# Optimization experiments

Measured on AMD Instinct MI355X. Metric: run time of the kernel, lower is better.

The kernel has to match this reference:

```python
import jax, jax.numpy as jnp
import numpy as np

N = 100000
HEADS = 4
NHID = 32


def _gat_conv(x, src, dst, W, a_src, a_dst, b):
    # x: [N, Fin]; src/dst: [E'] (self-loops already appended)
    h = (x @ W).reshape(N, HEADS, NHID)                      # [N, H, D]
    al_src = jnp.einsum('nhd,hd->nh', h, a_src)              # [N, H]
    al_dst = jnp.einsum('nhd,hd->nh', h, a_dst)
    e = jax.nn.leaky_relu(al_src[src] + al_dst[dst], 0.2)    # [E', H]
    # segment softmax over incoming edges of each destination node
    m = jax.ops.segment_max(e, dst, num_segments=N)          # [N, H]
    ex = jnp.exp(e - m[dst])
    s = jax.ops.segment_sum(ex, dst, num_segments=N)         # [N, H]
    alpha = ex / (s[dst] + 1e-16)                            # [E', H]
    msg = h[src] * alpha[:, :, None]                         # [E', H, D]
    out = jax.ops.segment_sum(msg, dst, num_segments=N)      # [N, H, D]
    return out.reshape(N, HEADS * NHID) + b


def setup_inputs() -> dict:
    key = jax.random.key(0)
    ks = jax.random.split(key, 16)
    E = 1600000
    NFEAT, NCLASS = 128, 10
    width = HEADS * NHID  # 128
    sc = 0.1
    inp = {
        'x': jax.random.normal(ks[0], (N, NFEAT), jnp.float32),
        'edge_index': jax.random.randint(ks[1], (2, E), 0, N, jnp.int64)
            if jax.config.jax_enable_x64 else jax.random.randint(ks[1], (2, E), 0, N, jnp.int32),
        'W0': jax.random.normal(ks[2], (NFEAT, width), jnp.float32) * sc,
        'a_src0': jax.random.normal(ks[3], (HEADS, NHID), jnp.float32) * sc,
        'a_dst0': jax.random.normal(ks[4], (HEADS, NHID), jnp.float32) * sc,
        'b0': jnp.zeros((width,), jnp.float32),
        'W1': jax.random.normal(ks[5], (width, width), jnp.float32) * sc,
        'a_src1': jax.random.normal(ks[6], (HEADS, NHID), jnp.float32) * sc,
        'a_dst1': jax.random.normal(ks[7], (HEADS, NHID), jnp.float32) * sc,
        'b1': jnp.zeros((width,), jnp.float32),
        'W2': jax.random.normal(ks[8], (width, width), jnp.float32) * sc,
        'a_src2': jax.random.normal(ks[9], (HEADS, NHID), jnp.float32) * sc,
        'a_dst2': jax.random.normal(ks[10], (HEADS, NHID), jnp.float32) * sc,
        'b2': jnp.zeros((width,), jnp.float32),
        'fc_W': jax.random.normal(ks[11], (width, NCLASS), jnp.float32) * sc,
        'fc_b': jnp.zeros((NCLASS,), jnp.float32),
    }
    return inp


def reference(x, edge_index, W0, a_src0, a_dst0, b0, W1, a_src1, a_dst1, b1,
              W2, a_src2, a_dst2, b2, fc_W, fc_b):
    # PyG GATConv default add_self_loops=True
    loops = jnp.arange(N, dtype=edge_index.dtype)
    src = jnp.concatenate([edge_index[0], loops])
    dst = jnp.concatenate([edge_index[1], loops])
    h = x
    for (W, a_s, a_d, b) in ((W0, a_src0, a_dst0, b0),
                             (W1, a_src1, a_dst1, b1),
                             (W2, a_src2, a_dst2, b2)):
        h = jax.nn.elu(_gat_conv(h, src, dst, W, a_s, a_d, b))
        # F.dropout(training=False) -> identity
    logits = h @ fc_W + fc_b
    return jax.nn.log_softmax(logits, axis=1)
```

## Files before the change

kernel.cpp:

```cpp
#include <hip/hip_runtime.h>
#include <math.h>

#define NN 100000
#define FEAT 128
#define NHEAD 4
#define BSH 9
#define BNODES 512
#define NBUCK 196
#define BCAP 16384
#define PA_EPT 16
#define GTILES 6250
#define HSTRIDE 136

typedef unsigned int uint;
typedef unsigned short ushort;
typedef __attribute__((ext_vector_type(8))) short short8;
typedef __attribute__((ext_vector_type(4))) float fx4;

__device__ __forceinline__ float lrelu(float v) { return v > 0.f ? v : 0.2f * v; }

__device__ __forceinline__ ushort f2bf(float f) {
    uint u = __float_as_uint(f);
    return (ushort)((u + 0x7fffu + ((u >> 16) & 1u)) >> 16);
}
__device__ __forceinline__ float bf_lo(uint u) { return __uint_as_float(u << 16); }
__device__ __forceinline__ float bf_hi(uint u) { return __uint_as_float(u & 0xffff0000u); }

__global__ __launch_bounds__(256) void convert_bf_kernel(
    const float* __restrict__ x, ushort* __restrict__ xbf)
{
    int i = blockIdx.x * 256 + threadIdx.x;
    if (i >= NN * FEAT / 4) return;
    float4 v = ((const float4*)x)[i];
    ushort4 u;
    u.x = f2bf(v.x); u.y = f2bf(v.y); u.z = f2bf(v.z); u.w = f2bf(v.w);
    ((ushort4*)xbf)[i] = u;
}

__global__ __launch_bounds__(256, 2) void gemm_mfma_kernel(
    const ushort* __restrict__ inbf, const float* __restrict__ W,
    const float* __restrict__ a_src, const float* __restrict__ a_dst,
    ushort* __restrict__ hbf, float* __restrict__ al_s, float* __restrict__ al_d)
{
    __shared__ __align__(16) ushort WA[FEAT * FEAT];
    __shared__ __align__(16) ushort HS[4][16 * HSTRIDE];
    const int t = threadIdx.x;
    for (int idx = t; idx < FEAT * FEAT; idx += 256) {
        int k = idx >> 7, m = idx & 127;
        int mt = m >> 4, kt = k >> 5, qq = (k >> 3) & 3, j = k & 7;
        int ln = qq * 16 + (m & 15);
        WA[((mt * 4 + kt) * 64 + ln) * 8 + j] = f2bf(W[idx]);
    }
    __syncthreads();

    const int wv = t >> 6, lane = t & 63;
    const int node_l = lane & 15, q = lane >> 4;

    short8 afr[8][4];
    #pragma unroll
    for (int mt = 0; mt < 8; ++mt)
        #pragma unroll
        for (int kt = 0; kt < 4; ++kt)
            afr[mt][kt] = *(const short8*)&WA[((mt * 4 + kt) * 64 + lane) * 8];

    const int stride = gridDim.x * 4;
    int tile = blockIdx.x * 4 + wv;
    if (tile >= GTILES) return;

    const ushort* rowp = inbf + (size_t)(tile * 16 + node_l) * FEAT + q * 8;
    short8 b0 = *(const short8*)(rowp);
    short8 b1 = *(const short8*)(rowp + 32);
    short8 b2 = *(const short8*)(rowp + 64);
    short8 b3 = *(const short8*)(rowp + 96);

    for (; tile < GTILES; tile += stride) {
        const int n0 = tile * 16;
        int ntile = tile + stride;
        short8 nb0, nb1, nb2, nb3;
        if (ntile < GTILES) {
            const ushort* nrp = inbf + (size_t)(ntile * 16 + node_l) * FEAT + q * 8;
            nb0 = *(const short8*)(nrp);
            nb1 = *(const short8*)(nrp + 32);
            nb2 = *(const short8*)(nrp + 64);
            nb3 = *(const short8*)(nrp + 96);
        }
        fx4 zero = {0.f, 0.f, 0.f, 0.f};
        fx4 acc[8];
        #pragma unroll
        for (int mt = 0; mt < 8; ++mt) acc[mt] = zero;
        #pragma unroll
        for (int kt = 0; kt < 4; ++kt) {
            short8 b = (kt == 0) ? b0 : (kt == 1) ? b1 : (kt == 2) ? b2 : b3;
            #pragma unroll
            for (int mt = 0; mt < 8; ++mt)
                acc[mt] = __builtin_amdgcn_mfma_f32_16x16x32_bf16(afr[mt][kt], b, acc[mt], 0, 0, 0);
        }
        float ps[4] = {0.f, 0.f, 0.f, 0.f};
        float pd[4] = {0.f, 0.f, 0.f, 0.f};
        #pragma unroll
        for (int mt = 0; mt < 8; ++mt) {
            float4 as4 = *(const float4*)(a_src + mt * 16 + q * 4);
            float4 ad4 = *(const float4*)(a_dst + mt * 16 + q * 4);
            ps[mt >> 1] += acc[mt][0] * as4.x + acc[mt][1] * as4.y + acc[mt][2] * as4.z + acc[mt][3] * as4.w;
            pd[mt >> 1] += acc[mt][0] * ad4.x + acc[mt][1] * ad4.y + acc[mt][2] * ad4.z + acc[mt][3] * ad4.w;
            ushort4 hv;
            hv.x = f2bf(acc[mt][0]); hv.y = f2bf(acc[mt][1]);
            hv.z = f2bf(acc[mt][2]); hv.w = f2bf(acc[mt][3]);
            *(ushort4*)&HS[wv][node_l * HSTRIDE + mt * 16 + q * 4] = hv;
        }
        #pragma unroll
        for (int h = 0; h < 4; ++h) {
            ps[h] += __shfl_xor(ps[h], 16); ps[h] += __shfl_xor(ps[h], 32);
            pd[h] += __shfl_xor(pd[h], 16); pd[h] += __shfl_xor(pd[h], 32);
        }
        float vs = (q == 0) ? ps[0] : (q == 1) ? ps[1] : (q == 2) ? ps[2] : ps[3];
        float vd = (q == 0) ? pd[0] : (q == 1) ? pd[1] : (q == 2) ? pd[2] : pd[3];
        al_s[(n0 + node_l) * 4 + q] = vs;
        al_d[(n0 + node_l) * 4 + q] = vd;
        #pragma unroll
        for (int it = 0; it < 4; ++it) {
            int fi = it * 64 + lane;
            int row = fi >> 4, colc = fi & 15;
            short8 v = *(const short8*)&HS[wv][row * HSTRIDE + colc * 8];
            *(short8*)(hbf + (size_t)n0 * FEAT + (size_t)fi * 8) = v;
        }
        b0 = nb0; b1 = nb1; b2 = nb2; b3 = nb3;
    }
}


__global__ void zero_small_kernel(int* bsize)
{
    int t = threadIdx.x;
    if (t < NBUCK) bsize[t] = 0;
}

__global__ __launch_bounds__(256) void bucket_hist_kernel(
    const int* __restrict__ ei, int E, int* bsize)
{
    __shared__ int lh[NBUCK];
    int t = threadIdx.x;
    if (t < NBUCK) lh[t] = 0;
    __syncthreads();
    int stride = gridDim.x * 256;
    for (int i = blockIdx.x * 256 + t; i < E + NN; i += stride) {
        int d = (i < E) ? ei[E + i] : (i - E);
        atomicAdd(&lh[d >> BSH], 1);
    }
    __syncthreads();
    if (t < NBUCK && lh[t]) atomicAdd(&bsize[t], lh[t]);
}

__global__ __launch_bounds__(256) void bucket_scan_kernel(
    const int* __restrict__ bsize, int* bbase, int* bcursor)
{
    __shared__ int sm[256];
    int t = threadIdx.x;
    int v = (t < NBUCK) ? bsize[t] : 0;
    sm[t] = v;
    __syncthreads();
    #pragma unroll
    for (int off = 1; off < 256; off <<= 1) {
        int x = (t >= off) ? sm[t - off] : 0;
        __syncthreads();
        sm[t] += x;
        __syncthreads();
    }
    if (t < NBUCK) {
        int excl = sm[t] - v;
        bbase[t] = excl;
        bcursor[t] = excl;
    }
    if (t == 255) bbase[NBUCK] = sm[255];
}

__global__ __launch_bounds__(256) void phaseA_bin_kernel(
    const int* __restrict__ ei, int E, int* bcursor, int2* __restrict__ pairs)
{
    __shared__ int lh[NBUCK], lb[NBUCK];
    int t = threadIdx.x;
    if (t < NBUCK) lh[t] = 0;
    __syncthreads();
    int base = blockIdx.x * (256 * PA_EPT) + t;
    int s[PA_EPT], d[PA_EPT];
    #pragma unroll
    for (int k = 0; k < PA_EPT; ++k) {
        int i = base + k * 256;
        if (i < E)            { s[k] = ei[i]; d[k] = ei[E + i]; }
        else if (i < E + NN)  { s[k] = i - E; d[k] = s[k]; }
        else                  { s[k] = 0; d[k] = -1; }
        if (d[k] >= 0) atomicAdd(&lh[d[k] >> BSH], 1);
    }
    __syncthreads();
    if (t < NBUCK) {
        int c = lh[t];
        lb[t] = c ? atomicAdd(&bcursor[t], c) : 0;
        lh[t] = 0;
    }
    __syncthreads();
    #pragma unroll
    for (int k = 0; k < PA_EPT; ++k) {
        if (d[k] >= 0) {
            int b = d[k] >> BSH;
            int off = atomicAdd(&lh[b], 1);
            pairs[lb[b] + off] = make_int2(d[k], s[k]);
        }
    }
}

__global__ __launch_bounds__(256) void phaseB_kernel(
    const int2* __restrict__ pairs, const int* __restrict__ bbase,
    int* __restrict__ row_ptr, int* __restrict__ colidx, int EP)
{
    __shared__ int nh[BNODES];
    __shared__ int ex[BNODES];
    __shared__ int ss[256];
    __shared__ int img[BCAP];
    int b = blockIdx.x, t = threadIdx.x;
    int node0 = b << BSH;
    int nend = min(NN - node0, BNODES);
    int pb = bbase[b], pe = bbase[b + 1];
    int span = pe - pb;
    for (int j = t; j < BNODES; j += 256) nh[j] = 0;
    __syncthreads();
    for (int i = t; i < span; i += 256)
        atomicAdd(&nh[pairs[pb + i].x - node0], 1);
    __syncthreads();
    int v0 = nh[2 * t], v1 = nh[2 * t + 1];
    int psc = v0 + v1;
    ss[t] = psc;
    __syncthreads();
    #pragma unroll
    for (int off = 1; off < 256; off <<= 1) {
        int x = (t >= off) ? ss[t - off] : 0;
        __syncthreads();
        ss[t] += x;
        __syncthreads();
    }
    int ep = ss[t] - psc;
    ex[2 * t] = ep;
    ex[2 * t + 1] = ep + v0;
    __syncthreads();
    for (int j = t; j < nend; j += 256) row_ptr[node0 + j] = pb + ex[j];
    if (b == NBUCK - 1 && t == 0) row_ptr[NN] = EP;
    for (int j = t; j < BNODES; j += 256) nh[j] = ex[j];
    __syncthreads();
    if (span <= BCAP) {
        for (int i = t; i < span; i += 256) {
            int2 p = pairs[pb + i];
            int pos = atomicAdd(&nh[p.x - node0], 1);
            img[pos] = p.y;
        }
        __syncthreads();
        for (int i = t; i < span; i += 256) colidx[pb + i] = img[i];
    } else {
        for (int i = t; i < span; i += 256) {
            int2 p = pairs[pb + i];
            int pos = atomicAdd(&nh[p.x - node0], 1);
            colidx[pb + pos] = p.y;
        }
    }
}

#define AGGR_STEP(hv, wgt)                                                    \
    a0 = fmaf(wgt, bf_lo(hv.x), a0); a1 = fmaf(wgt, bf_hi(hv.x), a1);        \
    a2 = fmaf(wgt, bf_lo(hv.y), a2); a3 = fmaf(wgt, bf_hi(hv.y), a3);        \
    a4 = fmaf(wgt, bf_lo(hv.z), a4); a5 = fmaf(wgt, bf_hi(hv.z), a5);        \
    a6 = fmaf(wgt, bf_lo(hv.w), a6); a7 = fmaf(wgt, bf_hi(hv.w), a7);

#define PROC4(cv)                                                             \
    {                                                                         \
        int s0 = cv.x, s1 = cv.y, s2 = cv.z, s3 = cv.w;                       \
        float w0 = __expf(lrelu(al_s[s0*4 + head] + ald_h));                  \
        float w1 = __expf(lrelu(al_s[s1*4 + head] + ald_h));                  \
        float w2 = __expf(lrelu(al_s[s2*4 + head] + ald_h));                  \
        float w3 = __expf(lrelu(al_s[s3*4 + head] + ald_h));                  \
        uint4 h0 = ((const uint4*)(hbf + (size_t)s0 * FEAT))[lane];           \
        uint4 h1 = ((const uint4*)(hbf + (size_t)s1 * FEAT))[lane];           \
        uint4 h2 = ((const uint4*)(hbf + (size_t)s2 * FEAT))[lane];           \
        uint4 h3 = ((const uint4*)(hbf + (size_t)s3 * FEAT))[lane];           \
        ssum += (w0 + w1) + (w2 + w3);                                        \
        AGGR_STEP(h0, w0) AGGR_STEP(h1, w1) AGGR_STEP(h2, w2) AGGR_STEP(h3, w3) \
    }

__global__ __launch_bounds__(256) void aggr_csr_kernel(
    const int* __restrict__ row_ptr, const int* __restrict__ colidx,
    const ushort* __restrict__ hbf, const float* __restrict__ al_s,
    const float* __restrict__ al_d, const float* __restrict__ bias,
    ushort* __restrict__ outbf)
{
    int t = threadIdx.x;
    int node = blockIdx.x * 16 + (t >> 4);
    if (node >= NN) return;
    int lane = t & 15;
    int head = lane >> 2;
    float ald_h = al_d[node * 4 + head];
    int beg = row_ptr[node], end = row_ptr[node + 1];

    float ssum = 0.f;
    float a0=0.f,a1=0.f,a2=0.f,a3=0.f,a4=0.f,a5=0.f,a6=0.f,a7=0.f;

    int p = beg;
    int4 ca;
    if (p + 4 <= end) ca = *(const int4*)&colidx[p];
    while (p + 8 <= end) {
        int4 na = *(const int4*)&colidx[p + 4];
        PROC4(ca)
        ca = na;
        p += 4;
    }
    if (p + 4 <= end) { PROC4(ca) p += 4; }
    for (; p < end; ++p) {
        int sn = colidx[p];
        float wq = __expf(lrelu(al_s[sn*4 + head] + ald_h));
        uint4 hv = ((const uint4*)(hbf + (size_t)sn * FEAT))[lane];
        ssum += wq;
        AGGR_STEP(hv, wq)
    }
    float inv = 1.f / (ssum + 1e-16f);
    const float* bp = bias + lane * 8;
    float o[8] = {a0,a1,a2,a3,a4,a5,a6,a7};
    #pragma unroll
    for (int k = 0; k < 8; ++k) {
        float v = o[k] * inv + bp[k];
        o[k] = v > 0.f ? v : __expf(v) - 1.f;
    }
    uint4 u;
    u.x = (uint)f2bf(o[0]) | ((uint)f2bf(o[1]) << 16);
    u.y = (uint)f2bf(o[2]) | ((uint)f2bf(o[3]) << 16);
    u.z = (uint)f2bf(o[4]) | ((uint)f2bf(o[5]) << 16);
    u.w = (uint)f2bf(o[6]) | ((uint)f2bf(o[7]) << 16);
    ((uint4*)(outbf + (size_t)node * FEAT))[lane] = u;
}

__global__ __launch_bounds__(256) void fc_kernel(
    const ushort* __restrict__ hbf, const float* __restrict__ fcW,
    const float* __restrict__ fcb, float* __restrict__ out)
{
    __shared__ float WT[10][FEAT];
    __shared__ float bl[10];
    int t = threadIdx.x;
    for (int i = t; i < FEAT * 10; i += 256) {
        int k = i / 10, c = i % 10;
        WT[c][k] = fcW[i];
    }
    if (t < 10) bl[t] = fcb[t];
    __syncthreads();
    int n = blockIdx.x * 256 + t;
    if (n >= NN) return;
    const uint4* row = (const uint4*)(hbf + (size_t)n * FEAT);
    float lg[10];
    #pragma unroll
    for (int c = 0; c < 10; ++c) lg[c] = bl[c];
    #pragma unroll 4
    for (int k8 = 0; k8 < 16; ++k8) {
        uint4 u = row[k8];
        float x0 = bf_lo(u.x), x1 = bf_hi(u.x), x2 = bf_lo(u.y), x3 = bf_hi(u.y);
        float x4 = bf_lo(u.z), x5 = bf_hi(u.z), x6 = bf_lo(u.w), x7 = bf_hi(u.w);
        #pragma unroll
        for (int c = 0; c < 10; ++c) {
            const float* wr = &WT[c][k8 * 8];
            float4 wa = *(const float4*)(wr);
            float4 wb = *(const float4*)(wr + 4);
            float acc = fmaf(x0, wa.x, fmaf(x1, wa.y, fmaf(x2, wa.z, x3 * wa.w)));
            acc = fmaf(x4, wb.x, fmaf(x5, wb.y, fmaf(x6, wb.z, fmaf(x7, wb.w, acc))));
            lg[c] += acc;
        }
    }
    float mx = lg[0];
    #pragma unroll
    for (int c = 1; c < 10; ++c) mx = fmaxf(mx, lg[c]);
    float se = 0.f;
    #pragma unroll
    for (int c = 0; c < 10; ++c) se += __expf(lg[c] - mx);
    float lse = mx + __logf(se);
    float2* op = (float2*)(out + (size_t)n * 10);
    #pragma unroll
    for (int c = 0; c < 5; ++c)
        op[c] = make_float2(lg[2*c] - lse, lg[2*c + 1] - lse);
}

extern "C" void kernel_launch(void* const* d_in, const int* in_sizes, int n_in,
                              void* d_out, int out_size, void* d_ws, size_t ws_size,
                              hipStream_t stream)
{
    const float* x   = (const float*)d_in[0];
    const int*   ei  = (const int*)d_in[1];
    const float* W[3]   = {(const float*)d_in[2], (const float*)d_in[6],  (const float*)d_in[10]};
    const float* asr[3] = {(const float*)d_in[3], (const float*)d_in[7],  (const float*)d_in[11]};
    const float* ads[3] = {(const float*)d_in[4], (const float*)d_in[8],  (const float*)d_in[12]};
    const float* bs[3]  = {(const float*)d_in[5], (const float*)d_in[9],  (const float*)d_in[13]};
    const float* fcW = (const float*)d_in[14];
    const float* fcb = (const float*)d_in[15];
    const int E  = in_sizes[1] / 2;
    const int EP = E + NN;

    ushort* xbf  = (ushort*)d_ws;
    ushort* hbf  = xbf + (size_t)NN * FEAT;
    ushort* ybf  = hbf + (size_t)NN * FEAT;
    float* als   = (float*)(ybf + (size_t)NN * FEAT);
    float* ald   = als + (size_t)NN * NHEAD;
    int* row_ptr = (int*)(ald + (size_t)NN * NHEAD);
    int* bsize   = row_ptr + NN + 1;
    int* bbase   = bsize + NBUCK;
    int* bcursor = bbase + NBUCK + 1;
    int2* pairs  = (int2*)(bcursor + NBUCK);
    int* colidx  = (int*)(pairs + (size_t)EP);

    zero_small_kernel<<<1, 256, 0, stream>>>(bsize);
    bucket_hist_kernel<<<1024, 256, 0, stream>>>(ei, E, bsize);
    bucket_scan_kernel<<<1, 256, 0, stream>>>(bsize, bbase, bcursor);
    phaseA_bin_kernel<<<(EP + 256*PA_EPT - 1) / (256*PA_EPT), 256, 0, stream>>>(ei, E, bcursor, pairs);
    phaseB_kernel<<<NBUCK, 256, 0, stream>>>(pairs, bbase, row_ptr, colidx, EP);

    convert_bf_kernel<<<(NN * FEAT / 4 + 255) / 256, 256, 0, stream>>>(x, xbf);

    const ushort* fin = xbf;
    for (int l = 0; l < 3; ++l) {
        gemm_mfma_kernel<<<512, 256, 0, stream>>>(fin, W[l], asr[l], ads[l], hbf, als, ald);
        aggr_csr_kernel<<<(NN + 15) / 16, 256, 0, stream>>>(row_ptr, colidx, hbf, als, ald, bs[l], ybf);
        fin = ybf;
    }
    fc_kernel<<<(NN + 255) / 256, 256, 0, stream>>>(ybf, fcW, fcb, (float*)d_out);
}
```

Measured before the change: 517.8 us.

## Fuse fp32-to-bf16 conversion into first GEMM and pack edge pairs into 32 bits

Removes the separate conversion kernel: the first-layer GEMM now reads fp32 input directly and packs it to bf16 in registers through a template flag. The binned edge pairs shrink from int2 to one packed uint holding the local destination (9 bits) and the source (17 bits), halving the pairs traffic in binning and CSR build. The software prefetch of the next tile's B fragments in the GEMM loop is also dropped, which may expose load latency. The packed encoding assumes node ids fit in 17 bits.

```diff
diff --git a/kernel.cpp b/kernel.cpp
--- a/kernel.cpp
+++ b/kernel.cpp
@@ -11,6 +11,7 @@
 #define PA_EPT 16
 #define GTILES 6250
 #define HSTRIDE 136
+#define SRCMASK 0x1FFFF
 
 typedef unsigned int uint;
 typedef unsigned short ushort;
@@ -26,19 +27,19 @@
 __device__ __forceinline__ float bf_lo(uint u) { return __uint_as_float(u << 16); }
 __device__ __forceinline__ float bf_hi(uint u) { return __uint_as_float(u & 0xffff0000u); }
 
-__global__ __launch_bounds__(256) void convert_bf_kernel(
-    const float* __restrict__ x, ushort* __restrict__ xbf)
-{
-    int i = blockIdx.x * 256 + threadIdx.x;
-    if (i >= NN * FEAT / 4) return;
-    float4 v = ((const float4*)x)[i];
-    ushort4 u;
-    u.x = f2bf(v.x); u.y = f2bf(v.y); u.z = f2bf(v.z); u.w = f2bf(v.w);
-    ((ushort4*)xbf)[i] = u;
-}
-
+__device__ __forceinline__ short8 pack8f(const float* p) {
+    float4 a = *(const float4*)p, b = *(const float4*)(p + 4);
+    short8 v;
+    v[0] = (short)f2bf(a.x); v[1] = (short)f2bf(a.y);
+    v[2] = (short)f2bf(a.z); v[3] = (short)f2bf(a.w);
+    v[4] = (short)f2bf(b.x); v[5] = (short)f2bf(b.y);
+    v[6] = (short)f2bf(b.z); v[7] = (short)f2bf(b.w);
+    return v;
+}
+
+template <bool FP32IN>
 __global__ __launch_bounds__(256, 2) void gemm_mfma_kernel(
-    const ushort* __restrict__ inbf, const float* __restrict__ W,
+    const void* __restrict__ in, const float* __restrict__ W,
     const float* __restrict__ a_src, const float* __restrict__ a_dst,
     ushort* __restrict__ hbf, float* __restrict__ al_s, float* __restrict__ al_d)
 {
@@ -63,26 +64,24 @@
         for (int kt = 0; kt < 4; ++kt)
             afr[mt][kt] = *(const short8*)&WA[((mt * 4 + kt) * 64 + lane) * 8];
 
-    const int stride = gridDim.x * 4;
-    int tile = blockIdx.x * 4 + wv;
-    if (tile >= GTILES) return;
-
-    const ushort* rowp = inbf + (size_t)(tile * 16 + node_l) * FEAT + q * 8;
-    short8 b0 = *(const short8*)(rowp);
-    short8 b1 = *(const short8*)(rowp + 32);
-    short8 b2 = *(const short8*)(rowp + 64);
-    short8 b3 = *(const short8*)(rowp + 96);
-
-    for (; tile < GTILES; tile += stride) {
+    const ushort* inbf = (const ushort*)in;
+    const float*  inf  = (const float*)in;
+
+    for (int tile = blockIdx.x * 4 + wv; tile < GTILES; tile += gridDim.x * 4) {
         const int n0 = tile * 16;
-        int ntile = tile + stride;
-        short8 nb0, nb1, nb2, nb3;
-        if (ntile < GTILES) {
-            const ushort* nrp = inbf + (size_t)(ntile * 16 + node_l) * FEAT + q * 8;
-            nb0 = *(const short8*)(nrp);
-            nb1 = *(const short8*)(nrp + 32);
-            nb2 = *(const short8*)(nrp + 64);
-            nb3 = *(const short8*)(nrp + 96);
+        short8 b0, b1, b2, b3;
+        if (FP32IN) {
+            const float* rf = inf + (size_t)(n0 + node_l) * FEAT + q * 8;
+            b0 = pack8f(rf);
+            b1 = pack8f(rf + 32);
+            b2 = pack8f(rf + 64);
+            b3 = pack8f(rf + 96);
+        } else {
+            const ushort* rowp = inbf + (size_t)(n0 + node_l) * FEAT + q * 8;
+            b0 = *(const short8*)(rowp);
+            b1 = *(const short8*)(rowp + 32);
+            b2 = *(const short8*)(rowp + 64);
+            b3 = *(const short8*)(rowp + 96);
         }
         fx4 zero = {0.f, 0.f, 0.f, 0.f};
         fx4 acc[8];
@@ -124,7 +123,6 @@
             short8 v = *(const short8*)&HS[wv][row * HSTRIDE + colc * 8];
             *(short8*)(hbf + (size_t)n0 * FEAT + (size_t)fi * 8) = v;
         }
-        b0 = nb0; b1 = nb1; b2 = nb2; b3 = nb3;
     }
 }
 
@@ -175,7 +173,7 @@
 }
 
 __global__ __launch_bounds__(256) void phaseA_bin_kernel(
-    const int* __restrict__ ei, int E, int* bcursor, int2* __restrict__ pairs)
+    const int* __restrict__ ei, int E, int* bcursor, uint* __restrict__ pairs)
 {
     __shared__ int lh[NBUCK], lb[NBUCK];
     int t = threadIdx.x;
@@ -203,13 +201,13 @@
         if (d[k] >= 0) {
             int b = d[k] >> BSH;
             int off = atomicAdd(&lh[b], 1);
-            pairs[lb[b] + off] = make_int2(d[k], s[k]);
+            pairs[lb[b] + off] = ((uint)(d[k] & (BNODES - 1)) << 17) | (uint)s[k];
         }
     }
 }
 
 __global__ __launch_bounds__(256) void phaseB_kernel(
-    const int2* __restrict__ pairs, const int* __restrict__ bbase,
+    const uint* __restrict__ pairs, const int* __restrict__ bbase,
     int* __restrict__ row_ptr, int* __restrict__ colidx, int EP)
 {
     __shared__ int nh[BNODES];
@@ -224,7 +222,7 @@
     for (int j = t; j < BNODES; j += 256) nh[j] = 0;
     __syncthreads();
     for (int i = t; i < span; i += 256)
-        atomicAdd(&nh[pairs[pb + i].x - node0], 1);
+        atomicAdd(&nh[pairs[pb + i] >> 17], 1);
     __syncthreads();
     int v0 = nh[2 * t], v1 = nh[2 * t + 1];
     int psc = v0 + v1;
@@ -247,17 +245,17 @@
     __syncthreads();
     if (span <= BCAP) {
         for (int i = t; i < span; i += 256) {
-            int2 p = pairs[pb + i];
-            int pos = atomicAdd(&nh[p.x - node0], 1);
-            img[pos] = p.y;
+            uint p = pairs[pb + i];
+            int pos = atomicAdd(&nh[p >> 17], 1);
+            img[pos] = (int)(p & SRCMASK);
         }
         __syncthreads();
         for (int i = t; i < span; i += 256) colidx[pb + i] = img[i];
     } else {
         for (int i = t; i < span; i += 256) {
-            int2 p = pairs[pb + i];
-            int pos = atomicAdd(&nh[p.x - node0], 1);
-            colidx[pb + pos] = p.y;
+            uint p = pairs[pb + i];
+            int pos = atomicAdd(&nh[p >> 17], 1);
+            colidx[pb + pos] = (int)(p & SRCMASK);
         }
     }
 }
@@ -395,8 +393,7 @@
     const int E  = in_sizes[1] / 2;
     const int EP = E + NN;
 
-    ushort* xbf  = (ushort*)d_ws;
-    ushort* hbf  = xbf + (size_t)NN * FEAT;
+    ushort* hbf  = (ushort*)d_ws;
     ushort* ybf  = hbf + (size_t)NN * FEAT;
     float* als   = (float*)(ybf + (size_t)NN * FEAT);
     float* ald   = als + (size_t)NN * NHEAD;
@@ -404,7 +401,7 @@
     int* bsize   = row_ptr + NN + 1;
     int* bbase   = bsize + NBUCK;
     int* bcursor = bbase + NBUCK + 1;
-    int2* pairs  = (int2*)(bcursor + NBUCK);
+    uint* pairs  = (uint*)(bcursor + NBUCK);
     int* colidx  = (int*)(pairs + (size_t)EP);
 
     zero_small_kernel<<<1, 256, 0, stream>>>(bsize);
@@ -413,13 +410,11 @@
     phaseA_bin_kernel<<<(EP + 256*PA_EPT - 1) / (256*PA_EPT), 256, 0, stream>>>(ei, E, bcursor, pairs);
     phaseB_kernel<<<NBUCK, 256, 0, stream>>>(pairs, bbase, row_ptr, colidx, EP);
 
-    convert_bf_kernel<<<(NN * FEAT / 4 + 255) / 256, 256, 0, stream>>>(x, xbf);
-
-    const ushort* fin = xbf;
-    for (int l = 0; l < 3; ++l) {
-        gemm_mfma_kernel<<<512, 256, 0, stream>>>(fin, W[l], asr[l], ads[l], hbf, als, ald);
+    gemm_mfma_kernel<true><<<512, 256, 0, stream>>>(x, W[0], asr[0], ads[0], hbf, als, ald);
+    aggr_csr_kernel<<<(NN + 15) / 16, 256, 0, stream>>>(row_ptr, colidx, hbf, als, ald, bs[0], ybf);
+    for (int l = 1; l < 3; ++l) {
+        gemm_mfma_kernel<false><<<512, 256, 0, stream>>>(ybf, W[l], asr[l], ads[l], hbf, als, ald);
         aggr_csr_kernel<<<(NN + 15) / 16, 256, 0, stream>>>(row_ptr, colidx, hbf, als, ald, bs[l], ybf);
-        fin = ybf;
     }
     fc_kernel<<<(NN + 255) / 256, 256, 0, stream>>>(ybf, fcW, fcb, (float*)d_out);
 }
```

Measured after the change: 493.7 us. 1.05x faster.
